# Kernel tuning notes

Measured on AMD Instinct MI355X. Metric: run time of the kernel, lower is better.

Reference implementation:

```python
import jax, jax.numpy as jnp
import numpy as np

B, S, D, H, HS = 2, 2048, 1024, 16, 64


def setup_inputs() -> dict:
    key = jax.random.key(0)
    ks = jax.random.split(key, 4)
    x = jax.random.normal(ks[0], (B, S, D), dtype=jnp.float32)
    # causal mask: 1.0 where key_pos <= query_pos, else 0.0
    mask = jnp.tril(jnp.ones((S, S), dtype=jnp.float32))
    w_qkv = jax.random.normal(ks[1], (D, 3, H, HS), dtype=jnp.float32) * 0.02
    b_qkv = jnp.zeros((3, H, HS), dtype=jnp.float32)
    w_proj = jax.random.normal(ks[2], (H, HS, D), dtype=jnp.float32) * 0.02
    b_proj = jnp.zeros((D,), dtype=jnp.float32)
    return {"x": x, "mask": mask, "w_qkv": w_qkv, "b_qkv": b_qkv,
            "w_proj": w_proj, "b_proj": b_proj}


def reference(x, mask, w_qkv, b_qkv, w_proj, b_proj):
    # c_attn: [B,S,D] @ [D,3,H,HS] -> [B,S,3,H,HS]
    qkv = jnp.einsum('bsd,dthc->bsthc', x, w_qkv) + b_qkv
    q, k, v = qkv[:, :, 0], qkv[:, :, 1], qkv[:, :, 2]  # [B,S,H,HS]
    scale = jax.lax.rsqrt(float(HS))
    q = q * scale
    # scores over head_size: [B,H,S(query),S(key)]
    scores = jnp.einsum('bqhc,bkhc->bhqk', q, k)
    scores = scores + (1.0 - mask) * -1e9
    weights = jax.nn.softmax(scores, axis=-1).astype(x.dtype)
    # attn_pdrop = 0.0 / inference: dropout is identity
    attn = jnp.einsum('bhqk,bkhc->bqhc', weights, v)  # [B,S,H,HS]
    out = jnp.einsum('bqhc,hcd->bqd', attn, w_proj) + b_proj
    return out
```

## Files before the change

kernel.cpp:

```cpp
#include <hip/hip_runtime.h>
#include <hip/hip_bf16.h>


#define Bb 2
#define Ss 2048
#define Dd 1024
#define Hh 16
#define HSs 64

typedef __bf16 bf16x8 __attribute__((ext_vector_type(8)));
typedef float  f32x4  __attribute__((ext_vector_type(4)));

__device__ __forceinline__ unsigned short f2bf(float f) {
  unsigned int u = __float_as_uint(f);
  unsigned int lsb = (u >> 16) & 1u;
  u += 0x7fffu + lsb;
  return (unsigned short)(u >> 16);
}

__device__ __forceinline__ void async16(const unsigned short* g, unsigned short* l) {
  __builtin_amdgcn_global_load_lds(
      (const __attribute__((address_space(1))) unsigned int*)g,
      (__attribute__((address_space(3))) unsigned int*)l,
      16, 0, 0);
}

__global__ __launch_bounds__(256) void k_cvt_bf16(const float* __restrict__ in,
                                                  unsigned short* __restrict__ out,
                                                  int n) {
  int i = (blockIdx.x * 256 + threadIdx.x) * 4;
  int stride = gridDim.x * 256 * 4;
  for (; i < n; i += stride) {
    float4 v = *reinterpret_cast<const float4*>(in + i);
    ushort4 o;
    o.x = f2bf(v.x); o.y = f2bf(v.y); o.z = f2bf(v.z); o.w = f2bf(v.w);
    *reinterpret_cast<ushort4*>(out + i) = o;
  }
}

__global__ __launch_bounds__(256) void k_transpose_bf16(const float* __restrict__ in,
                                                        unsigned short* __restrict__ out,
                                                        int R, int C) {
  __shared__ float t[32][33];
  int c0 = blockIdx.x * 32, r0 = blockIdx.y * 32;
  int tx = threadIdx.x, ty = threadIdx.y;
  #pragma unroll
  for (int i = 0; i < 32; i += 8)
    t[ty + i][tx] = in[(size_t)(r0 + ty + i) * C + (c0 + tx)];
  __syncthreads();
  #pragma unroll
  for (int i = 0; i < 32; i += 8)
    out[(size_t)(c0 + ty + i) * R + (r0 + tx)] = f2bf(t[tx][ty + i]);
}

__global__ __launch_bounds__(256) void k_gemm_qkv(const unsigned short* __restrict__ A,
                                                  const unsigned short* __restrict__ Bt,
                                                  const float* __restrict__ bias,
                                                  unsigned short* __restrict__ Qg,
                                                  unsigned short* __restrict__ Kg,
                                                  unsigned short* __restrict__ Vt) {
  __shared__ unsigned short S[2][128 * 64];
  const int K = 1024;
  int bid = blockIdx.x;
  int swz = (bid % 8) * 96 + bid / 8;
  int tm = swz / 24, tn = swz % 24;
  int m0 = tm * 128, n0 = tn * 128;
  int tid = threadIdx.x;
  int w = tid >> 6, l = tid & 63;
  int lr = l & 15, lg = l >> 4;
  int wm = (w >> 1) * 64, wn = (w & 1) * 64;
  int srow = l >> 3, scol = (l & 7) * 8;

  f32x4 acc[4][4];
  #pragma unroll
  for (int i = 0; i < 4; ++i)
    #pragma unroll
    for (int j = 0; j < 4; ++j)
      acc[i][j] = (f32x4){0.f, 0.f, 0.f, 0.f};

  for (int k0 = 0; k0 < K; k0 += 64) {
    #pragma unroll
    for (int c = 0; c < 4; ++c) {
      int chunk = w * 4 + c;
      int row = chunk * 8 + srow;
      async16(&A[(size_t)(m0 + row) * K + k0 + scol], &S[0][chunk * 512]);
      async16(&Bt[(size_t)(n0 + row) * K + k0 + scol], &S[1][chunk * 512]);
    }
    __syncthreads();
    #pragma unroll
    for (int kk = 0; kk < 64; kk += 32) {
      bf16x8 af[4], bfr[4];
      #pragma unroll
      for (int mf = 0; mf < 4; ++mf)
        af[mf] = *reinterpret_cast<const bf16x8*>(&S[0][(wm + mf * 16 + lr) * 64 + kk + lg * 8]);
      #pragma unroll
      for (int nf = 0; nf < 4; ++nf)
        bfr[nf] = *reinterpret_cast<const bf16x8*>(&S[1][(wn + nf * 16 + lr) * 64 + kk + lg * 8]);
      #pragma unroll
      for (int mf = 0; mf < 4; ++mf)
        #pragma unroll
        for (int nf = 0; nf < 4; ++nf)
          acc[mf][nf] = __builtin_amdgcn_mfma_f32_16x16x32_bf16(af[mf], bfr[nf], acc[mf][nf], 0, 0, 0);
    }
    __syncthreads();
  }

  if (n0 < 2048) {
    #pragma unroll
    for (int mf = 0; mf < 4; ++mf) {
      #pragma unroll
      for (int nf = 0; nf < 4; ++nf) {
        int n = n0 + wn + nf * 16 + lr;
        int t = n >> 10, r = n & 1023;
        int h = r >> 6, cc = r & 63;
        float bv = bias[n];
        #pragma unroll
        for (int j = 0; j < 4; ++j) {
          int m = m0 + wm + mf * 16 + lg * 4 + j;
          int b = m >> 11, s = m & 2047;
          size_t idx = ((size_t)(b * Hh + h) * Ss + s) * HSs + cc;
          float v = acc[mf][nf][j] + bv;
          if (t == 0) Qg[idx] = f2bf(v * 0.1803368801111244f);
          else        Kg[idx] = f2bf(v);
        }
      }
    }
  } else {
    unsigned short* Ts = &S[0][0];
    #pragma unroll
    for (int mf = 0; mf < 4; ++mf)
      #pragma unroll
      for (int nf = 0; nf < 4; ++nf) {
        int nl = wn + nf * 16 + lr;
        float bv = bias[n0 + nl];
        #pragma unroll
        for (int j = 0; j < 4; ++j) {
          int ml = wm + mf * 16 + lg * 4 + j;
          Ts[nl * 128 + (ml ^ ((nl & 7) << 3))] = f2bf(acc[mf][nf][j] + bv);
        }
      }
    __syncthreads();
    int nl = tid >> 1, mh = (tid & 1) * 64;
    int n = n0 + nl;
    int h = (n & 1023) >> 6, cc = n & 63;
    int bb = m0 >> 11, s0 = m0 & 2047;
    unsigned short* dst = &Vt[((size_t)(bb * Hh + h) * HSs + cc) * Ss + s0];
    #pragma unroll
    for (int i = 0; i < 8; ++i) {
      int m = mh + i * 8;
      bf16x8 v = *reinterpret_cast<const bf16x8*>(&Ts[nl * 128 + (m ^ ((nl & 7) << 3))]);
      *reinterpret_cast<bf16x8*>(&dst[m]) = v;
    }
  }
}

__global__ __launch_bounds__(256, 4) void k_attn(const unsigned short* __restrict__ Qg,
                                                 const unsigned short* __restrict__ Kg,
                                                 const unsigned short* __restrict__ Vt,
                                                 unsigned short* __restrict__ Ob) {
  __shared__ unsigned short Ks[2][64 * 64];
  __shared__ unsigned short Vs[2][64 * 64];
  __shared__ unsigned short Ps[4][16 * 64];

  int bid = blockIdx.x;
  int q = bid >> 5, bh = bid & 31;
  int b = bh >> 4, h = bh & 15;
  int qtA = q, qtB = 31 - q;
  int ntA = qtA + 1;

  int tid = threadIdx.x;
  int w = tid >> 6, l = tid & 63;
  int lr = l & 15, lg = l >> 4;
  int srow = l >> 3, scol = (l & 7) * 8;
  int swcol = scol ^ (srow << 3);

  const size_t kbase = (size_t)bh * Ss;
  const size_t vbase = (size_t)bh * HSs;

  int qt = qtA, qs0 = qtA * 64, qw = qs0 + w * 16;
  bf16x8 qf[2];
  #pragma unroll
  for (int kx = 0; kx < 2; ++kx)
    qf[kx] = *reinterpret_cast<const bf16x8*>(
        &Qg[(kbase + qw + lr) * HSs + kx * 32 + lg * 8]);

  f32x4 oacc[4];
  #pragma unroll
  for (int nf = 0; nf < 4; ++nf) oacc[nf] = (f32x4){0.f, 0.f, 0.f, 0.f};
  float mrun[4], lrun[4];
  #pragma unroll
  for (int j = 0; j < 4; ++j) { mrun[j] = -1e30f; lrun[j] = 0.f; }

  auto stage = [&](int tile, int buf) {
    #pragma unroll
    for (int cch = 0; cch < 2; ++cch) {
      int rr = w * 16 + cch * 8 + srow;
      async16(&Kg[(kbase + tile * 64 + rr) * HSs + swcol], &Ks[buf][(w * 2 + cch) * 512]);
      async16(&Vt[(vbase + rr) * Ss + tile * 64 + swcol], &Vs[buf][(w * 2 + cch) * 512]);
    }
  };

  auto writeO = [&]() {
    #pragma unroll
    for (int j = 0; j < 4; ++j) {
      float rinv = 1.0f / lrun[j];
      int s = qw + lg * 4 + j;
      #pragma unroll
      for (int nf = 0; nf < 4; ++nf) {
        int cc = nf * 16 + lr;
        Ob[((size_t)(b * Ss + s)) * Dd + h * HSs + cc] = f2bf(oacc[nf][j] * rinv);
      }
    }
  };

  stage(0, 0);

  for (int g = 0; g < 33; ++g) {
    __syncthreads();

    if (g + 1 < 33) {
      int nt = g + 1;
      int tile = (nt < ntA) ? nt : (nt - ntA);
      stage(tile, (g + 1) & 1);
    }

    if (g == ntA) {
      writeO();
      qt = qtB; qs0 = qtB * 64; qw = qs0 + w * 16;
      #pragma unroll
      for (int kx = 0; kx < 2; ++kx)
        qf[kx] = *reinterpret_cast<const bf16x8*>(
            &Qg[(kbase + qw + lr) * HSs + kx * 32 + lg * 8]);
      #pragma unroll
      for (int nf = 0; nf < 4; ++nf) oacc[nf] = (f32x4){0.f, 0.f, 0.f, 0.f};
      #pragma unroll
      for (int j = 0; j < 4; ++j) { mrun[j] = -1e30f; lrun[j] = 0.f; }
    }

    int t = (g < ntA) ? g : g - ntA;
    int cur = g & 1;

    f32x4 sacc[4];
    #pragma unroll
    for (int nf = 0; nf < 4; ++nf) sacc[nf] = (f32x4){0.f, 0.f, 0.f, 0.f};
    #pragma unroll
    for (int kx = 0; kx < 2; ++kx) {
      bf16x8 kf[4];
      #pragma unroll
      for (int nf = 0; nf < 4; ++nf)
        kf[nf] = *reinterpret_cast<const bf16x8*>(
            &Ks[cur][(nf * 16 + lr) * 64 + ((kx * 32 + lg * 8) ^ ((lr & 7) << 3))]);
      #pragma unroll
      for (int nf = 0; nf < 4; ++nf)
        sacc[nf] = __builtin_amdgcn_mfma_f32_16x16x32_bf16(qf[kx], kf[nf], sacc[nf], 0, 0, 0);
    }

    if (t == qt) {
      #pragma unroll
      for (int nf = 0; nf < 4; ++nf) {
        int kcol = t * 64 + nf * 16 + lr;
        #pragma unroll
        for (int j = 0; j < 4; ++j) {
          int qg2 = qw + lg * 4 + j;
          if (kcol > qg2) sacc[nf][j] = -1e30f;
        }
      }
    }

    float rmax[4];
    #pragma unroll
    for (int j = 0; j < 4; ++j) {
      float rm = fmaxf(fmaxf(sacc[0][j], sacc[1][j]), fmaxf(sacc[2][j], sacc[3][j]));
      #pragma unroll
      for (int d = 1; d < 16; d <<= 1)
        rm = fmaxf(rm, __shfl_xor(rm, d));
      rmax[j] = rm;
    }
    bool need = (rmax[0] > mrun[0] + 8.f) | (rmax[1] > mrun[1] + 8.f) |
                (rmax[2] > mrun[2] + 8.f) | (rmax[3] > mrun[3] + 8.f);
    if (__any(need)) {
      #pragma unroll
      for (int j = 0; j < 4; ++j) {
        float mnew = fmaxf(mrun[j], rmax[j]);
        float cf = exp2f(mrun[j] - mnew);
        mrun[j] = mnew;
        lrun[j] *= cf;
        #pragma unroll
        for (int nf = 0; nf < 4; ++nf)
          oacc[nf][j] *= cf;
      }
    }
    #pragma unroll
    for (int j = 0; j < 4; ++j) {
      float psum = 0.f;
      #pragma unroll
      for (int nf = 0; nf < 4; ++nf) {
        float pv = exp2f(sacc[nf][j] - mrun[j]);
        sacc[nf][j] = pv;
        psum += pv;
      }
      #pragma unroll
      for (int d = 1; d < 16; d <<= 1)
        psum += __shfl_xor(psum, d);
      lrun[j] += psum;
    }

    #pragma unroll
    for (int nf = 0; nf < 4; ++nf)
      #pragma unroll
      for (int j = 0; j < 4; ++j) {
        int prow = lg * 4 + j;
        Ps[w][prow * 64 + ((nf * 16 + lr) ^ ((prow & 7) << 3))] = f2bf(sacc[nf][j]);
      }

    #pragma unroll
    for (int kx = 0; kx < 2; ++kx) {
      bf16x8 pf = *reinterpret_cast<const bf16x8*>(
          &Ps[w][lr * 64 + ((kx * 32 + lg * 8) ^ ((lr & 7) << 3))]);
      bf16x8 vf[4];
      #pragma unroll
      for (int nf = 0; nf < 4; ++nf)
        vf[nf] = *reinterpret_cast<const bf16x8*>(
            &Vs[cur][(nf * 16 + lr) * 64 + ((kx * 32 + lg * 8) ^ ((lr & 7) << 3))]);
      #pragma unroll
      for (int nf = 0; nf < 4; ++nf)
        oacc[nf] = __builtin_amdgcn_mfma_f32_16x16x32_bf16(pf, vf[nf], oacc[nf], 0, 0, 0);
    }
  }

  writeO();
}

__global__ __launch_bounds__(256) void k_gemm_out(const unsigned short* __restrict__ A,
                                                  const unsigned short* __restrict__ Bt,
                                                  const float* __restrict__ bias,
                                                  float* __restrict__ Out) {
  __shared__ unsigned short As[128 * 64];
  __shared__ unsigned short Bs[128 * 64];
  const int K = 1024;
  int bid = blockIdx.x;
  int swz = (bid % 8) * 32 + bid / 8;
  int tm = swz / 8, tn = swz % 8;
  int m0 = tm * 128, n0 = tn * 128;
  int tid = threadIdx.x;
  int w = tid >> 6, l = tid & 63;
  int lr = l & 15, lg = l >> 4;
  int wm = (w >> 1) * 64, wn = (w & 1) * 64;
  int srow = l >> 3, scol = (l & 7) * 8;

  f32x4 acc[4][4];
  #pragma unroll
  for (int i = 0; i < 4; ++i)
    #pragma unroll
    for (int j = 0; j < 4; ++j)
      acc[i][j] = (f32x4){0.f, 0.f, 0.f, 0.f};

  for (int k0 = 0; k0 < K; k0 += 64) {
    #pragma unroll
    for (int c = 0; c < 4; ++c) {
      int chunk = w * 4 + c;
      int row = chunk * 8 + srow;
      async16(&A[(size_t)(m0 + row) * K + k0 + scol], &As[chunk * 512]);
      async16(&Bt[(size_t)(n0 + row) * K + k0 + scol], &Bs[chunk * 512]);
    }
    __syncthreads();
    #pragma unroll
    for (int kk = 0; kk < 64; kk += 32) {
      bf16x8 af[4], bfr[4];
      #pragma unroll
      for (int mf = 0; mf < 4; ++mf)
        af[mf] = *reinterpret_cast<const bf16x8*>(&As[(wm + mf * 16 + lr) * 64 + kk + lg * 8]);
      #pragma unroll
      for (int nf = 0; nf < 4; ++nf)
        bfr[nf] = *reinterpret_cast<const bf16x8*>(&Bs[(wn + nf * 16 + lr) * 64 + kk + lg * 8]);
      #pragma unroll
      for (int mf = 0; mf < 4; ++mf)
        #pragma unroll
        for (int nf = 0; nf < 4; ++nf)
          acc[mf][nf] = __builtin_amdgcn_mfma_f32_16x16x32_bf16(af[mf], bfr[nf], acc[mf][nf], 0, 0, 0);
    }
    __syncthreads();
  }

  #pragma unroll
  for (int mf = 0; mf < 4; ++mf)
    #pragma unroll
    for (int nf = 0; nf < 4; ++nf) {
      int n = n0 + wn + nf * 16 + lr;
      float bv = bias[n];
      #pragma unroll
      for (int j = 0; j < 4; ++j) {
        int m = m0 + wm + mf * 16 + lg * 4 + j;
        Out[(size_t)m * 1024 + n] = acc[mf][nf][j] + bv;
      }
    }
}

extern "C" void kernel_launch(void* const* d_in, const int* in_sizes, int n_in,
                              void* d_out, int out_size, void* d_ws, size_t ws_size,
                              hipStream_t stream) {
  (void)in_sizes; (void)n_in; (void)out_size; (void)ws_size;
  const float* x      = (const float*)d_in[0];
  const float* w_qkv  = (const float*)d_in[2];
  const float* b_qkv  = (const float*)d_in[3];
  const float* w_proj = (const float*)d_in[4];
  const float* b_proj = (const float*)d_in[5];
  float* out = (float*)d_out;

  char* ws = (char*)d_ws;
  unsigned short* xb    = (unsigned short*)(ws);
  unsigned short* wqkvT = (unsigned short*)(ws + 8388608);
  unsigned short* wpT   = (unsigned short*)(ws + 14680064);
  unsigned short* Qg    = (unsigned short*)(ws + 16777216);
  unsigned short* Kg    = (unsigned short*)(ws + 25165824);
  unsigned short* Vt    = (unsigned short*)(ws + 33554432);
  unsigned short* attnb = (unsigned short*)(ws + 41943040);

  k_cvt_bf16<<<dim3(2048), dim3(256), 0, stream>>>(x, xb, Bb * Ss * Dd);
  k_transpose_bf16<<<dim3(96, 32), dim3(32, 8), 0, stream>>>(w_qkv, wqkvT, 1024, 3072);
  k_transpose_bf16<<<dim3(32, 32), dim3(32, 8), 0, stream>>>(w_proj, wpT, 1024, 1024);
  k_gemm_qkv<<<dim3(32 * 24), dim3(256), 0, stream>>>(xb, wqkvT, b_qkv, Qg, Kg, Vt);
  k_attn<<<dim3(512), dim3(256), 0, stream>>>(Qg, Kg, Vt, attnb);
  k_gemm_out<<<dim3(32 * 8), dim3(256), 0, stream>>>(attnb, wpT, b_proj, out);
}
```

Baseline: 245.3 us.

## Share K/V tiles across two query tiles per block and transpose score MFMA

The attention kernel moves to 512 threads per block. Two adjacent query tiles per pair now share each staged K/V tile, so the block runs 34 iterations covering four query tiles, and a `t <= qt` guard skips tiles masked for one group. The score MFMA swaps operands so each lane owns one query row. That cuts the row max and sum reductions to two shuffles and allows packed bf16 conversion of P with v_cvt_pk_bf16_f32. The two weight transposes are merged into one launch. The cost is larger blocks with fewer per CU and some idle waves when a group has no work on a tile.

```diff
diff --git a/kernel.cpp b/kernel.cpp
--- a/kernel.cpp
+++ b/kernel.cpp
@@ -16,6 +16,12 @@
   unsigned int lsb = (u >> 16) & 1u;
   u += 0x7fffu + lsb;
   return (unsigned short)(u >> 16);
+}
+
+__device__ __forceinline__ unsigned int cvtpk(float lo, float hi) {
+  unsigned int r;
+  asm("v_cvt_pk_bf16_f32 %0, %1, %2" : "=v"(r) : "v"(lo), "v"(hi));
+  return r;
 }
 
 __device__ __forceinline__ void async16(const unsigned short* g, unsigned short* l) {
@@ -38,11 +44,16 @@
   }
 }
 
-__global__ __launch_bounds__(256) void k_transpose_bf16(const float* __restrict__ in,
-                                                        unsigned short* __restrict__ out,
-                                                        int R, int C) {
+__global__ __launch_bounds__(256) void k_transpose2(const float* __restrict__ wqkv,
+                                                    unsigned short* __restrict__ wqkvT,
+                                                    const float* __restrict__ wproj,
+                                                    unsigned short* __restrict__ wprojT) {
   __shared__ float t[32][33];
-  int c0 = blockIdx.x * 32, r0 = blockIdx.y * 32;
+  int bx = blockIdx.x;
+  const float* in; unsigned short* out; int R = 1024, C;
+  if (bx < 96) { in = wqkv; out = wqkvT; C = 3072; }
+  else         { in = wproj; out = wprojT; C = 1024; bx -= 96; }
+  int c0 = bx * 32, r0 = blockIdx.y * 32;
   int tx = threadIdx.x, ty = threadIdx.y;
   #pragma unroll
   for (int i = 0; i < 32; i += 8)
@@ -154,177 +165,178 @@
   }
 }
 
-__global__ __launch_bounds__(256, 4) void k_attn(const unsigned short* __restrict__ Qg,
+__global__ __launch_bounds__(512, 4) void k_attn(const unsigned short* __restrict__ Qg,
                                                  const unsigned short* __restrict__ Kg,
                                                  const unsigned short* __restrict__ Vt,
                                                  unsigned short* __restrict__ Ob) {
   __shared__ unsigned short Ks[2][64 * 64];
   __shared__ unsigned short Vs[2][64 * 64];
-  __shared__ unsigned short Ps[4][16 * 64];
+  __shared__ unsigned short Ps[8][16 * 64];
 
   int bid = blockIdx.x;
-  int q = bid >> 5, bh = bid & 31;
+  int p = bid >> 5, bh = bid & 31;
   int b = bh >> 4, h = bh & 15;
-  int qtA = q, qtB = 31 - q;
-  int ntA = qtA + 1;
 
   int tid = threadIdx.x;
   int w = tid >> 6, l = tid & 63;
+  int g = w >> 2;
   int lr = l & 15, lg = l >> 4;
+  int lg4 = lg * 4;
   int srow = l >> 3, scol = (l & 7) * 8;
   int swcol = scol ^ (srow << 3);
 
+  int qtA = 2 * p + g;
+  int qtB = 30 - 2 * p + g;
+  int ntA = 2 * p + 2;
+
   const size_t kbase = (size_t)bh * Ss;
   const size_t vbase = (size_t)bh * HSs;
 
-  int qt = qtA, qs0 = qtA * 64, qw = qs0 + w * 16;
+  int qt = qtA;
+  int qw0 = qtA * 64 + (w & 3) * 16;
   bf16x8 qf[2];
   #pragma unroll
   for (int kx = 0; kx < 2; ++kx)
     qf[kx] = *reinterpret_cast<const bf16x8*>(
-        &Qg[(kbase + qw + lr) * HSs + kx * 32 + lg * 8]);
+        &Qg[(kbase + qw0 + lr) * HSs + kx * 32 + lg * 8]);
 
   f32x4 oacc[4];
   #pragma unroll
   for (int nf = 0; nf < 4; ++nf) oacc[nf] = (f32x4){0.f, 0.f, 0.f, 0.f};
-  float mrun[4], lrun[4];
-  #pragma unroll
-  for (int j = 0; j < 4; ++j) { mrun[j] = -1e30f; lrun[j] = 0.f; }
+  float mrun = -1e30f, lrun = 0.f;
 
   auto stage = [&](int tile, int buf) {
-    #pragma unroll
-    for (int cch = 0; cch < 2; ++cch) {
-      int rr = w * 16 + cch * 8 + srow;
-      async16(&Kg[(kbase + tile * 64 + rr) * HSs + swcol], &Ks[buf][(w * 2 + cch) * 512]);
-      async16(&Vt[(vbase + rr) * Ss + tile * 64 + swcol], &Vs[buf][(w * 2 + cch) * 512]);
-    }
+    int rr = w * 8 + srow;
+    async16(&Kg[(kbase + tile * 64 + rr) * HSs + swcol], &Ks[buf][w * 512]);
+    async16(&Vt[(vbase + rr) * Ss + tile * 64 + swcol], &Vs[buf][w * 512]);
   };
 
   auto writeO = [&]() {
+    float rinv = 1.0f / lrun;
+    float rj[4];
+    #pragma unroll
+    for (int j = 0; j < 4; ++j) rj[j] = __shfl(rinv, lg4 + j);
     #pragma unroll
     for (int j = 0; j < 4; ++j) {
-      float rinv = 1.0f / lrun[j];
-      int s = qw + lg * 4 + j;
+      int s = qw0 + lg4 + j;
       #pragma unroll
       for (int nf = 0; nf < 4; ++nf) {
         int cc = nf * 16 + lr;
-        Ob[((size_t)(b * Ss + s)) * Dd + h * HSs + cc] = f2bf(oacc[nf][j] * rinv);
+        Ob[((size_t)(b * Ss + s)) * Dd + h * HSs + cc] = f2bf(oacc[nf][j] * rj[j]);
       }
     }
   };
 
   stage(0, 0);
 
-  for (int g = 0; g < 33; ++g) {
-    __syncthreads();
-
-    if (g + 1 < 33) {
-      int nt = g + 1;
+  for (int gi = 0; gi < 34; ++gi) {
+    __syncthreads();
+
+    if (gi + 1 < 34) {
+      int nt = gi + 1;
       int tile = (nt < ntA) ? nt : (nt - ntA);
-      stage(tile, (g + 1) & 1);
-    }
-
-    if (g == ntA) {
+      stage(tile, nt & 1);
+    }
+
+    if (gi == ntA) {
       writeO();
-      qt = qtB; qs0 = qtB * 64; qw = qs0 + w * 16;
+      qt = qtB; qw0 = qtB * 64 + (w & 3) * 16;
       #pragma unroll
       for (int kx = 0; kx < 2; ++kx)
         qf[kx] = *reinterpret_cast<const bf16x8*>(
-            &Qg[(kbase + qw + lr) * HSs + kx * 32 + lg * 8]);
+            &Qg[(kbase + qw0 + lr) * HSs + kx * 32 + lg * 8]);
       #pragma unroll
       for (int nf = 0; nf < 4; ++nf) oacc[nf] = (f32x4){0.f, 0.f, 0.f, 0.f};
-      #pragma unroll
-      for (int j = 0; j < 4; ++j) { mrun[j] = -1e30f; lrun[j] = 0.f; }
-    }
-
-    int t = (g < ntA) ? g : g - ntA;
-    int cur = g & 1;
-
-    f32x4 sacc[4];
-    #pragma unroll
-    for (int nf = 0; nf < 4; ++nf) sacc[nf] = (f32x4){0.f, 0.f, 0.f, 0.f};
-    #pragma unroll
-    for (int kx = 0; kx < 2; ++kx) {
-      bf16x8 kf[4];
+      mrun = -1e30f; lrun = 0.f;
+    }
+
+    int t = (gi < ntA) ? gi : gi - ntA;
+    int cur = gi & 1;
+
+    if (t <= qt) {
+      f32x4 sacc[4];
+      #pragma unroll
+      for (int nf = 0; nf < 4; ++nf) sacc[nf] = (f32x4){0.f, 0.f, 0.f, 0.f};
+      #pragma unroll
+      for (int kx = 0; kx < 2; ++kx) {
+        bf16x8 kf[4];
+        #pragma unroll
+        for (int nf = 0; nf < 4; ++nf)
+          kf[nf] = *reinterpret_cast<const bf16x8*>(
+              &Ks[cur][(nf * 16 + lr) * 64 + ((kx * 32 + lg * 8) ^ ((lr & 7) << 3))]);
+        #pragma unroll
+        for (int nf = 0; nf < 4; ++nf)
+          sacc[nf] = __builtin_amdgcn_mfma_f32_16x16x32_bf16(kf[nf], qf[kx], sacc[nf], 0, 0, 0);
+      }
+
+      if (t == qt) {
+        int qg2 = qw0 + lr;
+        #pragma unroll
+        for (int nf = 0; nf < 4; ++nf)
+          #pragma unroll
+          for (int j = 0; j < 4; ++j) {
+            int kg = t * 64 + nf * 16 + lg4 + j;
+            if (kg > qg2) sacc[nf][j] = -1e30f;
+          }
+      }
+
+      float rm = -1e30f;
       #pragma unroll
       for (int nf = 0; nf < 4; ++nf)
-        kf[nf] = *reinterpret_cast<const bf16x8*>(
-            &Ks[cur][(nf * 16 + lr) * 64 + ((kx * 32 + lg * 8) ^ ((lr & 7) << 3))]);
+        rm = fmaxf(rm, fmaxf(fmaxf(sacc[nf][0], sacc[nf][1]),
+                             fmaxf(sacc[nf][2], sacc[nf][3])));
+      rm = fmaxf(rm, __shfl_xor(rm, 16));
+      rm = fmaxf(rm, __shfl_xor(rm, 32));
+
+      if (__any(rm > mrun + 8.f)) {
+        float mnew = fmaxf(mrun, rm);
+        float cf = exp2f(mrun - mnew);
+        mrun = mnew; lrun *= cf;
+        float cj[4];
+        #pragma unroll
+        for (int j = 0; j < 4; ++j) cj[j] = __shfl(cf, lg4 + j);
+        #pragma unroll
+        for (int nf = 0; nf < 4; ++nf)
+          #pragma unroll
+          for (int j = 0; j < 4; ++j)
+            oacc[nf][j] *= cj[j];
+      }
+
+      float psum = 0.f;
       #pragma unroll
       for (int nf = 0; nf < 4; ++nf)
-        sacc[nf] = __builtin_amdgcn_mfma_f32_16x16x32_bf16(qf[kx], kf[nf], sacc[nf], 0, 0, 0);
-    }
-
-    if (t == qt) {
+        #pragma unroll
+        for (int j = 0; j < 4; ++j) {
+          float pv = exp2f(sacc[nf][j] - mrun);
+          sacc[nf][j] = pv;
+          psum += pv;
+        }
+      psum += __shfl_xor(psum, 16);
+      psum += __shfl_xor(psum, 32);
+      lrun += psum;
+
       #pragma unroll
       for (int nf = 0; nf < 4; ++nf) {
-        int kcol = t * 64 + nf * 16 + lr;
-        #pragma unroll
-        for (int j = 0; j < 4; ++j) {
-          int qg2 = qw + lg * 4 + j;
-          if (kcol > qg2) sacc[nf][j] = -1e30f;
-        }
-      }
-    }
-
-    float rmax[4];
-    #pragma unroll
-    for (int j = 0; j < 4; ++j) {
-      float rm = fmaxf(fmaxf(sacc[0][j], sacc[1][j]), fmaxf(sacc[2][j], sacc[3][j]));
-      #pragma unroll
-      for (int d = 1; d < 16; d <<= 1)
-        rm = fmaxf(rm, __shfl_xor(rm, d));
-      rmax[j] = rm;
-    }
-    bool need = (rmax[0] > mrun[0] + 8.f) | (rmax[1] > mrun[1] + 8.f) |
-                (rmax[2] > mrun[2] + 8.f) | (rmax[3] > mrun[3] + 8.f);
-    if (__any(need)) {
-      #pragma unroll
-      for (int j = 0; j < 4; ++j) {
-        float mnew = fmaxf(mrun[j], rmax[j]);
-        float cf = exp2f(mrun[j] - mnew);
-        mrun[j] = mnew;
-        lrun[j] *= cf;
-        #pragma unroll
-        for (int nf = 0; nf < 4; ++nf)
-          oacc[nf][j] *= cf;
-      }
-    }
-    #pragma unroll
-    for (int j = 0; j < 4; ++j) {
-      float psum = 0.f;
-      #pragma unroll
-      for (int nf = 0; nf < 4; ++nf) {
-        float pv = exp2f(sacc[nf][j] - mrun[j]);
-        sacc[nf][j] = pv;
-        psum += pv;
-      }
-      #pragma unroll
-      for (int d = 1; d < 16; d <<= 1)
-        psum += __shfl_xor(psum, d);
-      lrun[j] += psum;
-    }
-
-    #pragma unroll
-    for (int nf = 0; nf < 4; ++nf)
-      #pragma unroll
-      for (int j = 0; j < 4; ++j) {
-        int prow = lg * 4 + j;
-        Ps[w][prow * 64 + ((nf * 16 + lr) ^ ((prow & 7) << 3))] = f2bf(sacc[nf][j]);
-      }
-
-    #pragma unroll
-    for (int kx = 0; kx < 2; ++kx) {
-      bf16x8 pf = *reinterpret_cast<const bf16x8*>(
-          &Ps[w][lr * 64 + ((kx * 32 + lg * 8) ^ ((lr & 7) << 3))]);
-      bf16x8 vf[4];
-      #pragma unroll
-      for (int nf = 0; nf < 4; ++nf)
-        vf[nf] = *reinterpret_cast<const bf16x8*>(
-            &Vs[cur][(nf * 16 + lr) * 64 + ((kx * 32 + lg * 8) ^ ((lr & 7) << 3))]);
-      #pragma unroll
-      for (int nf = 0; nf < 4; ++nf)
-        oacc[nf] = __builtin_amdgcn_mfma_f32_16x16x32_bf16(pf, vf[nf], oacc[nf], 0, 0, 0);
+        uint2 pk;
+        pk.x = cvtpk(sacc[nf][0], sacc[nf][1]);
+        pk.y = cvtpk(sacc[nf][2], sacc[nf][3]);
+        int col = nf * 16 + lg4;
+        *reinterpret_cast<uint2*>(&Ps[w][lr * 64 + (col ^ ((lr & 7) << 3))]) = pk;
+      }
+
+      #pragma unroll
+      for (int kx = 0; kx < 2; ++kx) {
+        bf16x8 pf = *reinterpret_cast<const bf16x8*>(
+            &Ps[w][lr * 64 + ((kx * 32 + lg * 8) ^ ((lr & 7) << 3))]);
+        bf16x8 vf[4];
+        #pragma unroll
+        for (int nf = 0; nf < 4; ++nf)
+          vf[nf] = *reinterpret_cast<const bf16x8*>(
+              &Vs[cur][(nf * 16 + lr) * 64 + ((kx * 32 + lg * 8) ^ ((lr & 7) << 3))]);
+        #pragma unroll
+        for (int nf = 0; nf < 4; ++nf)
+          oacc[nf] = __builtin_amdgcn_mfma_f32_16x16x32_bf16(pf, vf[nf], oacc[nf], 0, 0, 0);
+      }
     }
   }
 
@@ -417,9 +429,8 @@
   unsigned short* attnb = (unsigned short*)(ws + 41943040);
 
   k_cvt_bf16<<<dim3(2048), dim3(256), 0, stream>>>(x, xb, Bb * Ss * Dd);
-  k_transpose_bf16<<<dim3(96, 32), dim3(32, 8), 0, stream>>>(w_qkv, wqkvT, 1024, 3072);
-  k_transpose_bf16<<<dim3(32, 32), dim3(32, 8), 0, stream>>>(w_proj, wpT, 1024, 1024);
+  k_transpose2<<<dim3(128, 32), dim3(32, 8), 0, stream>>>(w_qkv, wqkvT, w_proj, wpT);
   k_gemm_qkv<<<dim3(32 * 24), dim3(256), 0, stream>>>(xb, wqkvT, b_qkv, Qg, Kg, Vt);
-  k_attn<<<dim3(512), dim3(256), 0, stream>>>(Qg, Kg, Vt, attnb);
+  k_attn<<<dim3(512), dim3(512), 0, stream>>>(Qg, Kg, Vt, attnb);
   k_gemm_out<<<dim3(32 * 8), dim3(256), 0, stream>>>(attnb, wpT, b_proj, out);
 }
```

New measurement: 248.7 us. About the same (+1.4%).
